# Kernel optimization log

Measured on AMD Instinct MI355X. Metric: run time of the kernel, lower is better.

Reference implementation:

```python
import jax, jax.numpy as jnp
import numpy as np

NHID = 1024
HEADS = 16
SEQ = 2048
BATCH = 4


def gelu_bert(x):
    # paper variant: x * sigmoid(1.702 * x)
    return x * jax.nn.sigmoid(1.702 * x)


def setup_inputs() -> dict:
    key = jax.random.key(0)
    ks = jax.random.split(key, 20)
    s = 0.02
    inp = {
        "query": jax.random.normal(ks[0], (SEQ, BATCH, NHID), jnp.float32),
        "key": jax.random.normal(ks[1], (SEQ, BATCH, NHID), jnp.float32),
        "value": jax.random.normal(ks[2], (SEQ, BATCH, NHID), jnp.float32),
        # gating params (torch init is zeros/ones; randomize mildly for a nontrivial baseline)
        "qs_p": jax.random.normal(ks[3], (1, 1, NHID), jnp.float32) * s,
        "ks_p": jax.random.normal(ks[4], (1, 1, NHID), jnp.float32) * s,
        "vs_p": jax.random.normal(ks[5], (1, 1, NHID), jnp.float32) * s,
        # Overparam (vq): Linear(nhid, 2*nhid)
        "vq_w": jax.random.normal(ks[6], (2 * NHID, NHID), jnp.float32) * s,
        "vq_b": jax.random.normal(ks[7], (2 * NHID,), jnp.float32) * s,
        # q/k/v projections: Linear(nhid, nhid)
        "q_w": jax.random.normal(ks[8], (NHID, NHID), jnp.float32) * s,
        "q_b": jax.random.normal(ks[9], (NHID,), jnp.float32) * s,
        "k_w": jax.random.normal(ks[10], (NHID, NHID), jnp.float32) * s,
        "k_b": jax.random.normal(ks[11], (NHID,), jnp.float32) * s,
        "v_w": jax.random.normal(ks[12], (NHID, NHID), jnp.float32) * s,
        "v_b": jax.random.normal(ks[13], (NHID,), jnp.float32) * s,
        # residual gate: Linear(2*nhid, nhid)
        "r_w": jax.random.normal(ks[14], (NHID, 2 * NHID), jnp.float32) * s,
        "r_b": jax.random.normal(ks[15], (NHID,), jnp.float32) * s,
        "r_gate": jnp.ones((1, 1, NHID), jnp.float32),
    }
    return inp


def reference(query, key, value, qs_p, ks_p, vs_p, vq_w, vq_b,
              q_w, q_b, k_w, k_b, v_w, v_b, r_w, r_b, r_gate):
    dim = NHID // HEADS
    # sigmoid gates
    qs = jax.nn.sigmoid(qs_p)
    ksg = jax.nn.sigmoid(ks_p)
    vs0 = jax.nn.sigmoid(vs_p)
    # Overparam on vs: l1 -> split -> sigmoid(f) * tanh(c)
    cf = vs0 @ vq_w.T + vq_b           # [1,1,2*nhid]
    c, f = cf[..., :NHID], cf[..., NHID:]
    vs = jax.nn.sigmoid(f) * jnp.tanh(c)
    # linear projections
    query = query @ q_w.T + q_b
    key = key @ k_w.T + k_b
    value = value @ v_w.T + v_b
    # gated scaling
    q = qs * query                      # [S,B,nhid]
    k = ksg * key
    v = vs * value
    original_q = q
    # to batch-first, then split heads -> [B,H,S,d]
    def split_heads(x):
        x = jnp.transpose(x, (1, 0, 2))                 # [B,S,nhid]
        x = x.reshape(BATCH, -1, HEADS, dim)
        return jnp.transpose(x, (0, 2, 1, 3))           # [B,H,S,d]
    qh, kh, vh = split_heads(q), split_heads(k), split_heads(v)
    scores = jnp.einsum('bhqd,bhkd->bhqk', qh, kh) / jnp.sqrt(jnp.float32(dim))
    weights = jax.nn.softmax(scores, axis=-1)           # [B,H,Sq,Sk]
    mix = jnp.einsum('bhqk,bhkd->bhqd', weights, vh)    # [B,H,S,d]
    mix = jnp.transpose(mix, (0, 2, 1, 3)).reshape(BATCH, -1, NHID)  # [B,S,nhid]
    mix = jnp.transpose(mix, (1, 0, 2))                 # [S,B,nhid]
    # residual gate MLP
    rcat = jnp.concatenate([mix, original_q], axis=-1)  # [S,B,2*nhid]
    r = gelu_bert(rcat @ r_w.T + r_b)
    out = jax.nn.sigmoid(r_gate) * mix + r
    return out
```

## Files before the change

### kernel.cpp

```cpp
#include <hip/hip_runtime.h>
#include <hip/hip_bf16.h>
#include <math.h>

#define SEQ   2048
#define BATCH 4
#define NHID  1024
#define HEADS 16
#define DIM   64
#define MROWS (SEQ*BATCH)
#define LOG2E 1.44269504f

typedef __attribute__((ext_vector_type(8)))  short bf16x8;
typedef __attribute__((ext_vector_type(4)))  float f32x4;
typedef __attribute__((ext_vector_type(16))) float f32x16;

__device__ __forceinline__ float sigf(float x) { return 1.0f / (1.0f + expf(-x)); }

__device__ __forceinline__ unsigned short f2b(float x) {
    unsigned int u = __float_as_uint(x);
    return (unsigned short)((u + 0x7FFFu + ((u >> 16) & 1u)) >> 16);
}
__device__ __forceinline__ float b2f(unsigned short h) {
    return __uint_as_float(((unsigned int)h) << 16);
}
__device__ __forceinline__ unsigned pk2(float lo, float hi) {
    __hip_bfloat162 h = __float22bfloat162_rn(make_float2(lo, hi));
    union { __hip_bfloat162 h; unsigned u; } cv; cv.h = h;
    return cv.u;
}
__device__ __forceinline__ float fexp2(float x) {
    float tf = __builtin_fmaf(x, 8388608.0f, 1065103216.0f);
    return __uint_as_float((unsigned)(int)tf);
}
__device__ __forceinline__ void gload_lds16(const void* g, void* l) {
    __builtin_amdgcn_global_load_lds((const __attribute__((address_space(1))) void*)g,
                                     (__attribute__((address_space(3))) void*)l,
                                     16, 0, 0);
}

__global__ __launch_bounds__(256) void k_prep(const float* __restrict__ vs_p,
                                              const float* __restrict__ vq_w,
                                              const float* __restrict__ vq_b,
                                              float* __restrict__ cf,
                                              const float* __restrict__ s0,
                                              const float* __restrict__ s1,
                                              const float* __restrict__ s2,
                                              const float* __restrict__ s3,
                                              unsigned short* __restrict__ d0,
                                              unsigned short* __restrict__ d1,
                                              unsigned short* __restrict__ d2,
                                              unsigned short* __restrict__ d3)
{
    if (blockIdx.x < 512) {
        const int wave = threadIdx.x >> 6, lane = threadIdx.x & 63;
        const int j = blockIdx.x * 4 + wave;
        const float* w = vq_w + (size_t)j * NHID;
        float p = 0.f;
        for (int i = lane; i < NHID; i += 64) p += sigf(vs_p[i]) * w[i];
#pragma unroll
        for (int off = 32; off; off >>= 1) p += __shfl_down(p, off);
        if (lane == 0) cf[j] = p + vq_b[j];
        return;
    }
    int blk = blockIdx.x - 512;
    const float* src; unsigned short* dst;
    if      (blk < 1024) { src = s0; dst = d0; }
    else if (blk < 2048) { src = s1; dst = d1; blk -= 1024; }
    else if (blk < 3072) { src = s2; dst = d2; blk -= 2048; }
    else                 { src = s3; dst = d3; blk -= 3072; }
    const int i = (blk * 256 + threadIdx.x) * 4;
    float4 v = *(const float4*)(src + i);
    unsigned long long pack = (unsigned long long)f2b(v.x)
                            | ((unsigned long long)f2b(v.y) << 16)
                            | ((unsigned long long)f2b(v.z) << 32)
                            | ((unsigned long long)f2b(v.w) << 48);
    *(unsigned long long*)(dst + i) = pack;
}

__global__ __launch_bounds__(256) void k_scales(const float* __restrict__ qs_p,
                                                const float* __restrict__ ks_p,
                                                const float* __restrict__ r_gate,
                                                const float* __restrict__ cf,
                                                float* __restrict__ sq, float* __restrict__ sk,
                                                float* __restrict__ sv, float* __restrict__ rg)
{
    for (int n = threadIdx.x; n < NHID; n += 256) {
        sq[n] = sigf(qs_p[n]);
        sk[n] = sigf(ks_p[n]) * (0.125f * LOG2E);
        rg[n] = sigf(r_gate[n]);
        sv[n] = sigf(cf[n + NHID]) * tanhf(cf[n]);
    }
}

__global__ __launch_bounds__(256) void k_proj3(const float* __restrict__ A0,
                                               const float* __restrict__ A1,
                                               const float* __restrict__ A2,
                                               const unsigned short* __restrict__ W0,
                                               const unsigned short* __restrict__ W1,
                                               const unsigned short* __restrict__ W2,
                                               const float* __restrict__ b0,
                                               const float* __restrict__ b1,
                                               const float* __restrict__ b2,
                                               const float* __restrict__ c0,
                                               const float* __restrict__ c1,
                                               const float* __restrict__ c2,
                                               unsigned short* __restrict__ o0,
                                               unsigned short* __restrict__ o1,
                                               unsigned short* __restrict__ o2)
{
    __shared__ float          Asf[128 * 64];
    __shared__ unsigned short Bs[128 * 64];
    const int t = threadIdx.x;
    const int wid = t >> 6, lane = t & 63;
    const int wr = wid >> 1, wc = wid & 1;
    const int f = blockIdx.x;
    const int wg = (f & 7) * 192 + (f >> 3);
    const int seg = wg / 512, inner = wg - seg * 512;
    const int bm = inner >> 3, bn = inner & 7;
    const float* A = seg == 0 ? A0 : seg == 1 ? A1 : A2;
    const unsigned short* W = seg == 0 ? W0 : seg == 1 ? W1 : W2;
    const float* bias  = seg == 0 ? b0 : seg == 1 ? b1 : b2;
    const float* scale = seg == 0 ? c0 : seg == 1 ? c1 : c2;
    unsigned short* outb = seg == 0 ? o0 : seg == 1 ? o1 : o2;
    const float* Ab = A + (size_t)bm * 128 * NHID;
    const unsigned short* Bb = W + (size_t)bn * 128 * NHID;

    f32x4 acc[4][4] = {};

    for (int k0 = 0; k0 < NHID; k0 += 64) {
        __syncthreads();
#pragma unroll
        for (int it = 0; it < 8; ++it) {
            const int c   = it * 256 + t;
            const int row = c >> 4;
            const int g   = (c & 15) ^ (row & 15);
            gload_lds16(Ab + (size_t)row * NHID + k0 + g * 4, (char*)Asf + c * 16);
        }
#pragma unroll
        for (int it = 0; it < 4; ++it) {
            const int c   = it * 256 + t;
            const int row = c >> 3;
            const int g   = (c & 7) ^ (row & 7);
            gload_lds16(Bb + (size_t)row * NHID + k0 + g * 8, (char*)Bs + c * 16);
        }
        __syncthreads();
#pragma unroll
        for (int ks = 0; ks < 2; ++ks) {
            bf16x8 af[4], bf[4];
#pragma unroll
            for (int mi = 0; mi < 4; ++mi) {
                const int r   = wr * 64 + mi * 16 + (lane & 15);
                const int gc0 = ks * 8 + (lane >> 4) * 2;
                const int cl0 = gc0 ^ (r & 15);
                const int cl1 = (gc0 + 1) ^ (r & 15);
                f32x4 v0 = *(const f32x4*)&Asf[r * 64 + cl0 * 4];
                f32x4 v1 = *(const f32x4*)&Asf[r * 64 + cl1 * 4];
                union { unsigned w[4]; bf16x8 v; } pa;
                pa.w[0] = pk2(v0[0], v0[1]); pa.w[1] = pk2(v0[2], v0[3]);
                pa.w[2] = pk2(v1[0], v1[1]); pa.w[3] = pk2(v1[2], v1[3]);
                af[mi] = pa.v;
            }
#pragma unroll
            for (int ni = 0; ni < 4; ++ni) {
                const int r  = wc * 64 + ni * 16 + (lane & 15);
                const int c8 = (ks * 4 + (lane >> 4)) ^ (r & 7);
                bf[ni] = *(const bf16x8*)&Bs[r * 64 + c8 * 8];
            }
#pragma unroll
            for (int mi = 0; mi < 4; ++mi)
#pragma unroll
                for (int ni = 0; ni < 4; ++ni)
                    acc[mi][ni] = __builtin_amdgcn_mfma_f32_16x16x32_bf16(af[mi], bf[ni], acc[mi][ni], 0, 0, 0);
        }
    }

#pragma unroll
    for (int mi = 0; mi < 4; ++mi) {
#pragma unroll
        for (int r = 0; r < 4; ++r) {
            const int m = bm * 128 + wr * 64 + mi * 16 + (lane >> 4) * 4 + r;
#pragma unroll
            for (int ni = 0; ni < 4; ++ni) {
                const int n = bn * 128 + wc * 64 + ni * 16 + (lane & 15);
                const float v = scale[n] * (acc[mi][ni][r] + bias[n]);
                if (seg == 0) {
                    outb[(size_t)m * 2048 + 1024 + n] = f2b(v);
                } else {
                    const int s = m >> 2, b = m & 3, h = n >> 6, d = n & 63;
                    outb[((size_t)(b * HEADS + h) * SEQ + s) * DIM + d] = f2b(v);
                }
            }
        }
    }
}

__global__ __launch_bounds__(256) void k_final(const unsigned short* __restrict__ A,
                                               const unsigned short* __restrict__ W,
                                               const float* __restrict__ bias,
                                               const float* __restrict__ rg,
                                               float* __restrict__ outf,
                                               const unsigned short* __restrict__ mixb)
{
    __shared__ unsigned short As[128 * 64];
    __shared__ unsigned short Bs[128 * 64];
    const int t = threadIdx.x;
    const int wid = t >> 6, lane = t & 63;
    const int wr = wid >> 1, wc = wid & 1;
    int wg = blockIdx.y * 64 + blockIdx.x;
    wg = (wg & 7) * 64 + (wg >> 3);
    const int bm = wg >> 3, bn = wg & 7;
    const int K = 2 * NHID;
    const unsigned short* Ab = A + (size_t)bm * 128 * K;
    const unsigned short* Bb = W + (size_t)bn * 128 * K;

    f32x4 acc[4][4] = {};
    for (int k0 = 0; k0 < K; k0 += 64) {
        __syncthreads();
#pragma unroll
        for (int it = 0; it < 4; ++it) {
            const int c   = it * 256 + t;
            const int row = c >> 3;
            const int g8  = (c & 7) ^ (row & 7);
            gload_lds16(Ab + (size_t)row * K + k0 + g8 * 8, (char*)As + c * 16);
            gload_lds16(Bb + (size_t)row * K + k0 + g8 * 8, (char*)Bs + c * 16);
        }
        __syncthreads();
#pragma unroll
        for (int ks = 0; ks < 2; ++ks) {
            bf16x8 af[4], bf[4];
#pragma unroll
            for (int mi = 0; mi < 4; ++mi) {
                const int r  = wr * 64 + mi * 16 + (lane & 15);
                const int c8 = (ks * 4 + (lane >> 4)) ^ (r & 7);
                af[mi] = *(const bf16x8*)&As[r * 64 + c8 * 8];
            }
#pragma unroll
            for (int ni = 0; ni < 4; ++ni) {
                const int r  = wc * 64 + ni * 16 + (lane & 15);
                const int c8 = (ks * 4 + (lane >> 4)) ^ (r & 7);
                bf[ni] = *(const bf16x8*)&Bs[r * 64 + c8 * 8];
            }
#pragma unroll
            for (int mi = 0; mi < 4; ++mi)
#pragma unroll
                for (int ni = 0; ni < 4; ++ni)
                    acc[mi][ni] = __builtin_amdgcn_mfma_f32_16x16x32_bf16(af[mi], bf[ni], acc[mi][ni], 0, 0, 0);
        }
    }

#pragma unroll
    for (int mi = 0; mi < 4; ++mi) {
#pragma unroll
        for (int r = 0; r < 4; ++r) {
            const int m = bm * 128 + wr * 64 + mi * 16 + (lane >> 4) * 4 + r;
#pragma unroll
            for (int ni = 0; ni < 4; ++ni) {
                const int n = bn * 128 + wc * 64 + ni * 16 + (lane & 15);
                const float pre = acc[mi][ni][r] + bias[n];
                const float g = pre * sigf(1.702f * pre);
                const float mx = b2f(mixb[(size_t)m * 2048 + n]);
                outf[(size_t)m * NHID + n] = rg[n] * mx + g;
            }
        }
    }
}

__global__ __launch_bounds__(256) void k_vt(const unsigned short* __restrict__ Vin,
                                            unsigned short* __restrict__ Vout)
{
    __shared__ unsigned short Ls[64][66];
    const int bh = blockIdx.x >> 5, st = blockIdx.x & 31;
    const int t = threadIdx.x;
    const unsigned short* src = Vin + ((size_t)bh * SEQ + st * 64) * DIM;
    {
        const int s = t >> 2, d0 = (t & 3) * 16;
        *(bf16x8*)&Ls[s][d0]     = *(const bf16x8*)&src[s * DIM + d0];
        *(bf16x8*)&Ls[s][d0 + 8] = *(const bf16x8*)&src[s * DIM + d0 + 8];
    }
    __syncthreads();
    const int d = t >> 2, s0 = (t & 3) * 16;
    union { unsigned short h[16]; unsigned long long q[4]; } r;
#pragma unroll
    for (int i = 0; i < 16; ++i) r.h[i] = Ls[s0 + i][d];
    unsigned short* dst = Vout + ((size_t)bh * DIM + d) * SEQ + st * 64 + s0;
    *(unsigned long long*)&dst[0]  = r.q[0];
    *(unsigned long long*)&dst[8]  = r.q[1];
    *(unsigned long long*)&dst[4]  = r.q[2];
    *(unsigned long long*)&dst[12] = r.q[3];
}

#define LDS8(BASE, ROW, C8) \
    (*(const bf16x8*)&(BASE)[((ROW) << 6) + ((((C8) ^ ((ROW) & 7))) << 3)])

#define STAGE(KB, VB, J0) do {                                                   \
    _Pragma("unroll")                                                            \
    for (int it_ = 0; it_ < 2; ++it_) {                                          \
        const int ch_  = it_ * 256 + t;                                          \
        const int row_ = ch_ >> 3;                                               \
        const int c8_  = (ch_ & 7) ^ (row_ & 7);                                 \
        gload_lds16(Kbh + (size_t)((J0) + row_) * DIM + c8_ * 8,                 \
                    (char*)(KB) + ch_ * 16);                                     \
        gload_lds16(Vbh + (size_t)row_ * SEQ + (J0) + c8_ * 8,                   \
                    (char*)(VB) + ch_ * 16);                                     \
    }                                                                            \
} while (0)

#define TILE(KB, VB) do {                                                        \
    f32x16 sA = {}, sB = {};                                                     \
    __builtin_amdgcn_s_setprio(1);                                               \
    _Pragma("unroll")                                                            \
    for (int ds_ = 0; ds_ < 4; ++ds_) {                                          \
        bf16x8 kf0 = LDS8(KB, q31,      ds_ * 2 + g2);                           \
        bf16x8 kf1 = LDS8(KB, 32 + q31, ds_ * 2 + g2);                           \
        sA = __builtin_amdgcn_mfma_f32_32x32x16_bf16(kf0, qf[ds_], sA, 0, 0, 0); \
        sB = __builtin_amdgcn_mfma_f32_32x32x16_bf16(kf1, qf[ds_], sB, 0, 0, 0); \
    }                                                                            \
    __builtin_amdgcn_s_setprio(0);                                               \
    unsigned ppk[16];                                                            \
    _Pragma("unroll")                                                            \
    for (int p = 0; p < 8; ++p) {                                                \
        ppk[p]     = pk2(fexp2(sA[2 * p]), fexp2(sA[2 * p + 1]));                \
        ppk[8 + p] = pk2(fexp2(sB[2 * p]), fexp2(sB[2 * p + 1]));                \
    }                                                                            \
    f32x16 accP = {};                                                            \
    __builtin_amdgcn_s_setprio(1);                                               \
    _Pragma("unroll")                                                            \
    for (int kc = 0; kc < 4; ++kc) {                                             \
        union { unsigned w[4]; bf16x8 v; } up;                                   \
        up.w[0] = ppk[4 * kc + 0];                                               \
        up.w[1] = ppk[4 * kc + 1];                                               \
        up.w[2] = ppk[4 * kc + 2];                                               \
        up.w[3] = ppk[4 * kc + 3];                                               \
        bf16x8 vf0 = LDS8(VB, q31,      kc * 2 + g2);                            \
        bf16x8 vf1 = LDS8(VB, 32 + q31, kc * 2 + g2);                            \
        accP  = __builtin_amdgcn_mfma_f32_32x32x16_bf16(aone.v, up.v, accP, 0, 0, 0);\
        accO0 = __builtin_amdgcn_mfma_f32_32x32x16_bf16(vf0, up.v, accO0, 0, 0, 0);\
        accO1 = __builtin_amdgcn_mfma_f32_32x32x16_bf16(vf1, up.v, accO1, 0, 0, 0);\
    }                                                                            \
    __builtin_amdgcn_s_setprio(0);                                               \
    l_r += accP[0];                                                              \
} while (0)

__global__ __launch_bounds__(256, 4) void k_attn(const unsigned short* __restrict__ Qc,
                                                 const unsigned short* __restrict__ Kb,
                                                 const unsigned short* __restrict__ Vt,
                                                 unsigned short* __restrict__ mixo)
{
    __shared__ unsigned short Ks0[4096], Ks1[4096];
    __shared__ unsigned short Vs0[4096], Vs1[4096];
    const int t = threadIdx.x, wid = t >> 6, l = t & 63;
    const int g2 = l >> 5, q31 = l & 31;
    const int f = blockIdx.x;
    const int bh = (f & 7) + ((f >> 7) << 3);
    const int qt = (f >> 3) & 15;
    const int b = bh >> 4, h = bh & 15;
    const int s_q = qt * 128 + wid * 32 + q31;

    const unsigned short* Kbh = Kb + (size_t)bh * SEQ * DIM;
    const unsigned short* Vbh = Vt + (size_t)bh * DIM * SEQ;
    const unsigned short* Qrow = Qc + (size_t)(s_q * 4 + b) * 2048 + 1024 + h * 64;

    bf16x8 qf[4];
#pragma unroll
    for (int ds_ = 0; ds_ < 4; ++ds_)
        qf[ds_] = *(const bf16x8*)&Qrow[ds_ * 16 + g2 * 8];

    union { unsigned w[4]; bf16x8 v; } aone;
    aone.w[0] = aone.w[1] = aone.w[2] = aone.w[3] = 0x3F803F80u;

    f32x16 accO0 = {}, accO1 = {};
    float l_r = 0.f;

    STAGE(Ks0, Vs0, 0);
#pragma unroll 1
    for (int j0 = 0; j0 < SEQ; j0 += 128) {
        __syncthreads();
        if (j0 + 64 < SEQ) STAGE(Ks1, Vs1, j0 + 64);
        TILE(Ks0, Vs0);
        __syncthreads();
        if (j0 + 128 < SEQ) STAGE(Ks0, Vs0, j0 + 128);
        TILE(Ks1, Vs1);
    }

    const float inv = 1.f / l_r;
    unsigned short* dst = mixo + (size_t)(s_q * 4 + b) * 2048 + h * 64;
#pragma unroll
    for (int reg = 0; reg < 16; reg += 2) {
        const int d0a = (reg & 3) + 8 * (reg >> 2) + 4 * g2;
        *(unsigned*)&dst[d0a]      = pk2(accO0[reg] * inv, accO0[reg + 1] * inv);
        *(unsigned*)&dst[32 + d0a] = pk2(accO1[reg] * inv, accO1[reg + 1] * inv);
    }
}

extern "C" void kernel_launch(void* const* d_in, const int* in_sizes, int n_in,
                              void* d_out, int out_size, void* d_ws, size_t ws_size,
                              hipStream_t stream)
{
    (void)in_sizes; (void)n_in; (void)out_size; (void)ws_size;
    const float* query  = (const float*)d_in[0];
    const float* key    = (const float*)d_in[1];
    const float* value  = (const float*)d_in[2];
    const float* qs_p   = (const float*)d_in[3];
    const float* ks_p   = (const float*)d_in[4];
    const float* vs_p   = (const float*)d_in[5];
    const float* vq_w   = (const float*)d_in[6];
    const float* vq_b   = (const float*)d_in[7];
    const float* q_w    = (const float*)d_in[8];
    const float* q_b    = (const float*)d_in[9];
    const float* k_w    = (const float*)d_in[10];
    const float* k_b    = (const float*)d_in[11];
    const float* v_w    = (const float*)d_in[12];
    const float* v_b    = (const float*)d_in[13];
    const float* r_w    = (const float*)d_in[14];
    const float* r_b    = (const float*)d_in[15];
    const float* r_gate = (const float*)d_in[16];

    float* fws = (float*)d_ws;
    float* sq = fws;
    float* sk = fws + 1024;
    float* sv = fws + 2048;
    float* rg = fws + 3072;
    float* cf = fws + 4096;

    unsigned short* uws = (unsigned short*)(fws + 8192);
    unsigned short* Wq = uws;
    unsigned short* Wk = Wq + (size_t)NHID * NHID;
    unsigned short* Wv = Wk + (size_t)NHID * NHID;
    unsigned short* Wr = Wv + (size_t)NHID * NHID;
    unsigned short* Qc = Wr + (size_t)NHID * 2 * NHID;
    unsigned short* Kb = Qc + (size_t)MROWS * 2 * NHID;
    unsigned short* Vb = Kb + (size_t)BATCH * HEADS * SEQ * DIM;
    unsigned short* Vtmp = Vb + (size_t)BATCH * HEADS * SEQ * DIM;

    k_prep<<<dim3(5632), dim3(256), 0, stream>>>(vs_p, vq_w, vq_b, cf,
                                                 q_w, k_w, v_w, r_w,
                                                 Wq, Wk, Wv, Wr);
    k_scales<<<dim3(1), dim3(256), 0, stream>>>(qs_p, ks_p, r_gate, cf, sq, sk, sv, rg);

    k_proj3<<<dim3(1536), dim3(256), 0, stream>>>(query, key, value, Wq, Wk, Wv,
                                                  q_b, k_b, v_b, sq, sk, sv,
                                                  Qc, Kb, Vtmp);
    k_vt<<<dim3(2048), dim3(256), 0, stream>>>(Vtmp, Vb);

    k_attn<<<dim3(1024), dim3(256), 0, stream>>>(Qc, Kb, Vb, Qc);

    k_final<<<dim3(64, 8), dim3(256), 0, stream>>>(Qc, Wr, r_b, rg, (float*)d_out, Qc);
}
```

Baseline: 268.0 us.

## Pre-convert activations to bf16 and fuse V transpose into projection epilogue

The prep kernel now also converts the query, key and value activations to bf16. The projection GEMM can then stage bf16 A tiles directly, instead of loading fp32 and packing to bf16 inside the inner loop. The V projection's epilogue writes its result transposed through shared memory straight into the [B,H,D,S] layout, which removes the separate k_vt kernel and its intermediate buffer. In exchange, the activations take an extra full read and write pass through global memory in the prep kernel.

Result: faster. 256.4 us (-4.3%).

```diff
diff --git a/kernel.cpp b/kernel.cpp
--- a/kernel.cpp
+++ b/kernel.cpp
@@ -46,10 +46,16 @@
                                               const float* __restrict__ s1,
                                               const float* __restrict__ s2,
                                               const float* __restrict__ s3,
+                                              const float* __restrict__ s4,
+                                              const float* __restrict__ s5,
+                                              const float* __restrict__ s6,
                                               unsigned short* __restrict__ d0,
                                               unsigned short* __restrict__ d1,
                                               unsigned short* __restrict__ d2,
-                                              unsigned short* __restrict__ d3)
+                                              unsigned short* __restrict__ d3,
+                                              unsigned short* __restrict__ d4,
+                                              unsigned short* __restrict__ d5,
+                                              unsigned short* __restrict__ d6)
 {
     if (blockIdx.x < 512) {
         const int wave = threadIdx.x >> 6, lane = threadIdx.x & 63;
@@ -64,10 +70,13 @@
     }
     int blk = blockIdx.x - 512;
     const float* src; unsigned short* dst;
-    if      (blk < 1024) { src = s0; dst = d0; }
-    else if (blk < 2048) { src = s1; dst = d1; blk -= 1024; }
-    else if (blk < 3072) { src = s2; dst = d2; blk -= 2048; }
-    else                 { src = s3; dst = d3; blk -= 3072; }
+    if      (blk < 8192)  { src = s0; dst = d0; }
+    else if (blk < 16384) { src = s1; dst = d1; blk -= 8192;  }
+    else if (blk < 24576) { src = s2; dst = d2; blk -= 16384; }
+    else if (blk < 25600) { src = s3; dst = d3; blk -= 24576; }
+    else if (blk < 26624) { src = s4; dst = d4; blk -= 25600; }
+    else if (blk < 27648) { src = s5; dst = d5; blk -= 26624; }
+    else                  { src = s6; dst = d6; blk -= 27648; }
     const int i = (blk * 256 + threadIdx.x) * 4;
     float4 v = *(const float4*)(src + i);
     unsigned long long pack = (unsigned long long)f2b(v.x)
@@ -92,9 +101,9 @@
     }
 }
 
-__global__ __launch_bounds__(256) void k_proj3(const float* __restrict__ A0,
-                                               const float* __restrict__ A1,
-                                               const float* __restrict__ A2,
+__global__ __launch_bounds__(256) void k_proj3(const unsigned short* __restrict__ A0,
+                                               const unsigned short* __restrict__ A1,
+                                               const unsigned short* __restrict__ A2,
                                                const unsigned short* __restrict__ W0,
                                                const unsigned short* __restrict__ W1,
                                                const unsigned short* __restrict__ W2,
@@ -108,8 +117,9 @@
                                                unsigned short* __restrict__ o1,
                                                unsigned short* __restrict__ o2)
 {
-    __shared__ float          Asf[128 * 64];
-    __shared__ unsigned short Bs[128 * 64];
+    __shared__ char smem[33280];
+    unsigned short* As = (unsigned short*)smem;
+    unsigned short* Bs = (unsigned short*)(smem + 16384);
     const int t = threadIdx.x;
     const int wid = t >> 6, lane = t & 63;
     const int wr = wid >> 1, wc = wid & 1;
@@ -117,31 +127,24 @@
     const int wg = (f & 7) * 192 + (f >> 3);
     const int seg = wg / 512, inner = wg - seg * 512;
     const int bm = inner >> 3, bn = inner & 7;
-    const float* A = seg == 0 ? A0 : seg == 1 ? A1 : A2;
+    const unsigned short* A = seg == 0 ? A0 : seg == 1 ? A1 : A2;
     const unsigned short* W = seg == 0 ? W0 : seg == 1 ? W1 : W2;
     const float* bias  = seg == 0 ? b0 : seg == 1 ? b1 : b2;
     const float* scale = seg == 0 ? c0 : seg == 1 ? c1 : c2;
-    unsigned short* outb = seg == 0 ? o0 : seg == 1 ? o1 : o2;
-    const float* Ab = A + (size_t)bm * 128 * NHID;
+    const unsigned short* Ab = A + (size_t)bm * 128 * NHID;
     const unsigned short* Bb = W + (size_t)bn * 128 * NHID;
 
     f32x4 acc[4][4] = {};
 
     for (int k0 = 0; k0 < NHID; k0 += 64) {
         __syncthreads();
-#pragma unroll
-        for (int it = 0; it < 8; ++it) {
-            const int c   = it * 256 + t;
-            const int row = c >> 4;
-            const int g   = (c & 15) ^ (row & 15);
-            gload_lds16(Ab + (size_t)row * NHID + k0 + g * 4, (char*)Asf + c * 16);
-        }
 #pragma unroll
         for (int it = 0; it < 4; ++it) {
             const int c   = it * 256 + t;
             const int row = c >> 3;
-            const int g   = (c & 7) ^ (row & 7);
-            gload_lds16(Bb + (size_t)row * NHID + k0 + g * 8, (char*)Bs + c * 16);
+            const int g8  = (c & 7) ^ (row & 7);
+            gload_lds16(Ab + (size_t)row * NHID + k0 + g8 * 8, (char*)As + c * 16);
+            gload_lds16(Bb + (size_t)row * NHID + k0 + g8 * 8, (char*)Bs + c * 16);
         }
         __syncthreads();
 #pragma unroll
@@ -149,16 +152,9 @@
             bf16x8 af[4], bf[4];
 #pragma unroll
             for (int mi = 0; mi < 4; ++mi) {
-                const int r   = wr * 64 + mi * 16 + (lane & 15);
-                const int gc0 = ks * 8 + (lane >> 4) * 2;
-                const int cl0 = gc0 ^ (r & 15);
-                const int cl1 = (gc0 + 1) ^ (r & 15);
-                f32x4 v0 = *(const f32x4*)&Asf[r * 64 + cl0 * 4];
-                f32x4 v1 = *(const f32x4*)&Asf[r * 64 + cl1 * 4];
-                union { unsigned w[4]; bf16x8 v; } pa;
-                pa.w[0] = pk2(v0[0], v0[1]); pa.w[1] = pk2(v0[2], v0[3]);
-                pa.w[2] = pk2(v1[0], v1[1]); pa.w[3] = pk2(v1[2], v1[3]);
-                af[mi] = pa.v;
+                const int r  = wr * 64 + mi * 16 + (lane & 15);
+                const int c8 = (ks * 4 + (lane >> 4)) ^ (r & 7);
+                af[mi] = *(const bf16x8*)&As[r * 64 + c8 * 8];
             }
 #pragma unroll
             for (int ni = 0; ni < 4; ++ni) {
@@ -174,22 +170,60 @@
         }
     }
 
+    if (seg < 2) {
+        unsigned short* outb = seg == 0 ? o0 : o1;
+#pragma unroll
+        for (int mi = 0; mi < 4; ++mi) {
+#pragma unroll
+            for (int r = 0; r < 4; ++r) {
+                const int m = bm * 128 + wr * 64 + mi * 16 + (lane >> 4) * 4 + r;
+#pragma unroll
+                for (int ni = 0; ni < 4; ++ni) {
+                    const int n = bn * 128 + wc * 64 + ni * 16 + (lane & 15);
+                    const float v = scale[n] * (acc[mi][ni][r] + bias[n]);
+                    if (seg == 0) {
+                        outb[(size_t)m * 2048 + 1024 + n] = f2b(v);
+                    } else {
+                        const int s = m >> 2, b = m & 3, h = n >> 6, d = n & 63;
+                        outb[((size_t)(b * HEADS + h) * SEQ + s) * DIM + d] = f2b(v);
+                    }
+                }
+            }
+        }
+        return;
+    }
+
+    unsigned short* L = (unsigned short*)smem;
+    __syncthreads();
 #pragma unroll
     for (int mi = 0; mi < 4; ++mi) {
 #pragma unroll
         for (int r = 0; r < 4; ++r) {
-            const int m = bm * 128 + wr * 64 + mi * 16 + (lane >> 4) * 4 + r;
+            const int ml = wr * 64 + mi * 16 + (lane >> 4) * 4 + r;
 #pragma unroll
             for (int ni = 0; ni < 4; ++ni) {
-                const int n = bn * 128 + wc * 64 + ni * 16 + (lane & 15);
-                const float v = scale[n] * (acc[mi][ni][r] + bias[n]);
-                if (seg == 0) {
-                    outb[(size_t)m * 2048 + 1024 + n] = f2b(v);
-                } else {
-                    const int s = m >> 2, b = m & 3, h = n >> 6, d = n & 63;
-                    outb[((size_t)(b * HEADS + h) * SEQ + s) * DIM + d] = f2b(v);
-                }
-            }
+                const int nl = wc * 64 + ni * 16 + (lane & 15);
+                const int n = bn * 128 + nl;
+                L[nl * 130 + ml] = f2b(scale[n] * (acc[mi][ni][r] + bias[n]));
+            }
+        }
+    }
+    __syncthreads();
+    const int hl = t >> 7, d = (t >> 1) & 63, half = t & 1;
+    const int nlr = hl * 64 + d;
+    const int sl0 = half * 16;
+#pragma unroll
+    for (int b = 0; b < 4; ++b) {
+        unsigned short* dst = o2 + ((size_t)((b * HEADS) + 2 * bn + hl) * DIM + d) * SEQ
+                            + bm * 32 + sl0;
+#pragma unroll
+        for (int q = 0; q < 4; ++q) {
+            union { unsigned short h[4]; unsigned long long u; } pk;
+#pragma unroll
+            for (int j = 0; j < 4; ++j)
+                pk.h[j] = L[nlr * 130 + (sl0 + q * 4 + j) * 4 + b];
+            const int po = (q == 1) ? 8 : (q == 2) ? 4 : (q == 3) ? 12 : 0;
+            *(unsigned long long*)&dst[po] = pk.u;
         }
     }
 }
@@ -263,30 +297,6 @@
             }
         }
     }
-}
-
-__global__ __launch_bounds__(256) void k_vt(const unsigned short* __restrict__ Vin,
-                                            unsigned short* __restrict__ Vout)
-{
-    __shared__ unsigned short Ls[64][66];
-    const int bh = blockIdx.x >> 5, st = blockIdx.x & 31;
-    const int t = threadIdx.x;
-    const unsigned short* src = Vin + ((size_t)bh * SEQ + st * 64) * DIM;
-    {
-        const int s = t >> 2, d0 = (t & 3) * 16;
-        *(bf16x8*)&Ls[s][d0]     = *(const bf16x8*)&src[s * DIM + d0];
-        *(bf16x8*)&Ls[s][d0 + 8] = *(const bf16x8*)&src[s * DIM + d0 + 8];
-    }
-    __syncthreads();
-    const int d = t >> 2, s0 = (t & 3) * 16;
-    union { unsigned short h[16]; unsigned long long q[4]; } r;
-#pragma unroll
-    for (int i = 0; i < 16; ++i) r.h[i] = Ls[s0 + i][d];
-    unsigned short* dst = Vout + ((size_t)bh * DIM + d) * SEQ + st * 64 + s0;
-    *(unsigned long long*)&dst[0]  = r.q[0];
-    *(unsigned long long*)&dst[8]  = r.q[1];
-    *(unsigned long long*)&dst[4]  = r.q[2];
-    *(unsigned long long*)&dst[12] = r.q[3];
 }
 
 #define LDS8(BASE, ROW, C8) \
@@ -423,24 +433,26 @@
     float* cf = fws + 4096;
 
     unsigned short* uws = (unsigned short*)(fws + 8192);
-    unsigned short* Wq = uws;
+    unsigned short* Xq = uws;
+    unsigned short* Xk = Xq + (size_t)MROWS * NHID;
+    unsigned short* Xv = Xk + (size_t)MROWS * NHID;
+    unsigned short* Wq = Xv + (size_t)MROWS * NHID;
     unsigned short* Wk = Wq + (size_t)NHID * NHID;
     unsigned short* Wv = Wk + (size_t)NHID * NHID;
     unsigned short* Wr = Wv + (size_t)NHID * NHID;
     unsigned short* Qc = Wr + (size_t)NHID * 2 * NHID;
     unsigned short* Kb = Qc + (size_t)MROWS * 2 * NHID;
     unsigned short* Vb = Kb + (size_t)BATCH * HEADS * SEQ * DIM;
-    unsigned short* Vtmp = Vb + (size_t)BATCH * HEADS * SEQ * DIM;
-
-    k_prep<<<dim3(5632), dim3(256), 0, stream>>>(vs_p, vq_w, vq_b, cf,
-                                                 q_w, k_w, v_w, r_w,
-                                                 Wq, Wk, Wv, Wr);
+
+    k_prep<<<dim3(30208), dim3(256), 0, stream>>>(vs_p, vq_w, vq_b, cf,
+                                                  query, key, value,
+                                                  q_w, k_w, v_w, r_w,
+                                                  Xq, Xk, Xv, Wq, Wk, Wv, Wr);
     k_scales<<<dim3(1), dim3(256), 0, stream>>>(qs_p, ks_p, r_gate, cf, sq, sk, sv, rg);
 
-    k_proj3<<<dim3(1536), dim3(256), 0, stream>>>(query, key, value, Wq, Wk, Wv,
+    k_proj3<<<dim3(1536), dim3(256), 0, stream>>>(Xq, Xk, Xv, Wq, Wk, Wv,
                                                   q_b, k_b, v_b, sq, sk, sv,
-                                                  Qc, Kb, Vtmp);
-    k_vt<<<dim3(2048), dim3(256), 0, stream>>>(Vtmp, Vb);
+                                                  Qc, Kb, Vb);
 
     k_attn<<<dim3(1024), dim3(256), 0, stream>>>(Qc, Kb, Vb, Qc);
 
```
